# Performance work log

Measured on AMD Instinct MI355X. Metric: run time of the kernel, lower is better.

The kernel has to match this reference:

```python
import jax, jax.numpy as jnp
import numpy as np

B, S, D = 1, 4096, 1024
H = 16
HD = D // H  # 64


def setup_inputs() -> dict:
    key = jax.random.key(0)
    k1, k2, k3 = jax.random.split(key, 3)
    x = jax.random.normal(k1, (B, S, D), dtype=jnp.float32)
    W_qkv = jax.random.normal(k2, (D, 3 * D), dtype=jnp.float32) * (1.0 / np.sqrt(D))
    b_qkv = jnp.zeros((3 * D,), dtype=jnp.float32)
    W_out = jax.random.normal(k3, (D, D), dtype=jnp.float32) * (1.0 / np.sqrt(D))
    b_out = jnp.zeros((D,), dtype=jnp.float32)
    return {"x": x, "W_qkv": W_qkv, "b_qkv": b_qkv, "W_out": W_out, "b_out": b_out}


def reference(x, W_qkv, b_qkv, W_out, b_out):
    b, s, d = x.shape
    qkv = x @ W_qkv + b_qkv                      # [b, s, 3d]
    q, k, v = jnp.split(qkv, 3, axis=-1)
    q = q.reshape(b, s, H, HD)
    k = k.reshape(b, s, H, HD)
    v = v.reshape(b, s, H, HD)
    scale = 1.0 / np.sqrt(HD).astype(np.float32)
    scores = jnp.einsum("bqhd,bkhd->bhqk", q, k) * scale  # [b, h, s, s]
    causal = jnp.tril(jnp.ones((s, s), dtype=bool))
    scores = jnp.where(causal, scores, jnp.float32(-jnp.inf))
    attn = jax.nn.softmax(scores, axis=-1)
    out = jnp.einsum("bhqk,bkhd->bqhd", attn, v).reshape(b, s, d)
    return out @ W_out + b_out
```

## Files before the change

kernel.cpp:

```cpp
#include <hip/hip_runtime.h>
#include <cstdint>
#include <cstddef>


typedef __attribute__((ext_vector_type(4))) float f32x4;
typedef __attribute__((ext_vector_type(16))) float f32x16;
typedef __attribute__((ext_vector_type(8))) short s16x8;
typedef __attribute__((ext_vector_type(4))) unsigned u32x4;

#define SM_SCALE_LOG2 0.18033688011112042f

#if __has_builtin(__builtin_amdgcn_exp2f)
#define EXP2(x) __builtin_amdgcn_exp2f(x)
#else
#define EXP2(x) exp2f(x)
#endif

static __device__ __forceinline__ short f2bf(float f) {
  unsigned u = __builtin_bit_cast(unsigned, f);
  u = (u + 0x7fffu + ((u >> 16) & 1u)) >> 16;
  return (short)u;
}

static __device__ __forceinline__ unsigned cvtpk(float lo, float hi) {
  unsigned r;
  asm("v_cvt_pk_bf16_f32 %0, %1, %2" : "=v"(r) : "v"(lo), "v"(hi));
  return r;
}

static __device__ __forceinline__ void plswap(unsigned& a, unsigned& b) {
#if __has_builtin(__builtin_amdgcn_permlane32_swap)
  auto r = __builtin_amdgcn_permlane32_swap((int)a, (int)b, false, false);
  unsigned tmp[2];
  __builtin_memcpy(tmp, &r, 8);
  a = tmp[0];
  b = tmp[1];
#else
  const unsigned xa = (unsigned)__shfl_xor((int)a, 32);
  const unsigned xb = (unsigned)__shfl_xor((int)b, 32);
  const bool hiL = (threadIdx.x & 32) != 0;
  const unsigned na = hiL ? xb : a;
  const unsigned nb = hiL ? b : xa;
  a = na;
  b = nb;
#endif
}

static __device__ __forceinline__ void gload16(const void* g, void* l) {
  __builtin_amdgcn_global_load_lds((const __attribute__((address_space(1))) void*)g,
                                   (__attribute__((address_space(3))) void*)l, 16, 0, 0);
}

#define MFMA32(A, B, C) __builtin_amdgcn_mfma_f32_32x32x16_bf16(A, B, C, 0, 0, 0)

__global__ __launch_bounds__(256) void convx_k(const float* __restrict__ x,
                                               short* __restrict__ xb) {
  const size_t i = ((size_t)blockIdx.x * 256 + threadIdx.x) * 8;
  float4 a = *(const float4*)(x + i);
  float4 b = *(const float4*)(x + i + 4);
  u32x4 p;
  p[0] = cvtpk(a.x, a.y); p[1] = cvtpk(a.z, a.w);
  p[2] = cvtpk(b.x, b.y); p[3] = cvtpk(b.z, b.w);
  *(u32x4*)(xb + i) = p;
}

__global__ __launch_bounds__(256, 2) void convT_k(const float* __restrict__ W,
                                                  short* __restrict__ Wt, int K, int N) {
  __shared__ short T[64][72];
  const int t = threadIdx.x;
  const int n0 = blockIdx.x * 64, k0 = blockIdx.y * 64;
  const int kr = t >> 2, c0 = (t & 3) * 16;
  const float* src = W + (size_t)(k0 + kr) * N + n0 + c0;
  float4 v0 = *(const float4*)(src + 0);
  float4 v1 = *(const float4*)(src + 4);
  float4 v2 = *(const float4*)(src + 8);
  float4 v3 = *(const float4*)(src + 12);
  T[c0 + 0][kr] = f2bf(v0.x);  T[c0 + 1][kr] = f2bf(v0.y);
  T[c0 + 2][kr] = f2bf(v0.z);  T[c0 + 3][kr] = f2bf(v0.w);
  T[c0 + 4][kr] = f2bf(v1.x);  T[c0 + 5][kr] = f2bf(v1.y);
  T[c0 + 6][kr] = f2bf(v1.z);  T[c0 + 7][kr] = f2bf(v1.w);
  T[c0 + 8][kr] = f2bf(v2.x);  T[c0 + 9][kr] = f2bf(v2.y);
  T[c0 + 10][kr] = f2bf(v2.z); T[c0 + 11][kr] = f2bf(v2.w);
  T[c0 + 12][kr] = f2bf(v3.x); T[c0 + 13][kr] = f2bf(v3.y);
  T[c0 + 14][kr] = f2bf(v3.z); T[c0 + 15][kr] = f2bf(v3.w);
  __syncthreads();
  const int nr = t >> 2, kc = (t & 3) * 16;
  s16x8 a = *(const s16x8*)&T[nr][kc];
  s16x8 b = *(const s16x8*)&T[nr][kc + 8];
  short* dst = Wt + (size_t)(n0 + nr) * K + k0 + kc;
  *(s16x8*)dst = a;
  *(s16x8*)(dst + 8) = b;
}

template <int ABF, int SCAT>
__global__ __launch_bounds__(256, 2) void gemm_k(
    const void* __restrict__ Ap, const short* __restrict__ Bt,
    const float* __restrict__ bias,
    short* __restrict__ q_ws, short* __restrict__ k_ws, short* __restrict__ vt_ws,
    float* __restrict__ out, int N, int K) {
  constexpr int LDA = ABF ? 32 : 40;
  __shared__ short As[2][128 * LDA];
  __shared__ short Bs[2][128 * 32];

  const int t = threadIdx.x, l = t & 63, w = t >> 6;
  const int wm = (w >> 1) * 64, wn = (w & 1) * 64;
  const int m0 = blockIdx.x * 128, n0 = blockIdx.y * 128;
  const int lr = l & 15, lh = l >> 4;

  f32x4 acc[4][4];
#pragma unroll
  for (int i = 0; i < 4; i++)
#pragma unroll
    for (int j = 0; j < 4; j++) acc[i][j] = (f32x4){0.f, 0.f, 0.f, 0.f};

  const int arow = t >> 1, ac0 = (t & 1) * 16;
  const int grow = l >> 2, gc0 = (l & 3) * 8;

  auto stage = [&](int b, int kt) {
    {
      const int r0 = w * 32;
      const short* s0 = Bt + (size_t)(n0 + r0 + grow) * K + kt + gc0;
      gload16(s0, &Bs[b][r0 * 32]);
      gload16(s0 + (size_t)16 * K, &Bs[b][(r0 + 16) * 32]);
    }
    if constexpr (ABF) {
      const int r0 = w * 32;
      const short* s0 = (const short*)Ap + (size_t)(m0 + r0 + grow) * K + kt + gc0;
      gload16(s0, &As[b][r0 * 32]);
      gload16(s0 + (size_t)16 * K, &As[b][(r0 + 16) * 32]);
    } else {
      const float* ap = (const float*)Ap + (size_t)(m0 + arow) * K + kt + ac0;
      float4 v0 = *(const float4*)(ap + 0);
      float4 v1 = *(const float4*)(ap + 4);
      float4 v2 = *(const float4*)(ap + 8);
      float4 v3 = *(const float4*)(ap + 12);
      u32x4 p0, p1;
      p0[0] = cvtpk(v0.x, v0.y); p0[1] = cvtpk(v0.z, v0.w);
      p0[2] = cvtpk(v1.x, v1.y); p0[3] = cvtpk(v1.z, v1.w);
      p1[0] = cvtpk(v2.x, v2.y); p1[1] = cvtpk(v2.z, v2.w);
      p1[2] = cvtpk(v3.x, v3.y); p1[3] = cvtpk(v3.z, v3.w);
      *(u32x4*)&As[b][arow * LDA + ac0] = p0;
      *(u32x4*)&As[b][arow * LDA + ac0 + 8] = p1;
    }
  };

  const int nt = K >> 5;
  stage(0, 0);
  __syncthreads();
  int cur = 0;
  for (int tt = 0; tt < nt; tt++) {
    if (tt + 1 < nt) stage(cur ^ 1, (tt + 1) * 32);
    s16x8 af[4], bfv[4];
#pragma unroll
    for (int mi = 0; mi < 4; mi++)
      af[mi] = *(const s16x8*)&As[cur][(wm + mi * 16 + lr) * LDA + lh * 8];
#pragma unroll
    for (int ni = 0; ni < 4; ni++)
      bfv[ni] = *(const s16x8*)&Bs[cur][(wn + ni * 16 + lr) * 32 + lh * 8];
#pragma unroll
    for (int mi = 0; mi < 4; mi++)
#pragma unroll
      for (int ni = 0; ni < 4; ni++)
        acc[mi][ni] = __builtin_amdgcn_mfma_f32_16x16x32_bf16(af[mi], bfv[ni],
                                                              acc[mi][ni], 0, 0, 0);
    __syncthreads();
    cur ^= 1;
  }

#pragma unroll
  for (int mi = 0; mi < 4; mi++) {
#pragma unroll
    for (int ni = 0; ni < 4; ni++) {
      const int gn = n0 + wn + ni * 16 + lr;
      const float bb = bias[gn];
      if constexpr (SCAT) {
        const int sect = gn >> 10, dd = gn & 1023, hh = dd >> 6, hd = dd & 63;
#pragma unroll
        for (int j = 0; j < 4; j++) {
          const int gm = m0 + wm + mi * 16 + lh * 4 + j;
          const short bv = f2bf(acc[mi][ni][j] + bb);
          if (sect == 0)
            q_ws[((size_t)hh * 4096 + gm) * 64 + hd] = bv;
          else if (sect == 1)
            k_ws[((size_t)hh * 4096 + gm) * 64 + (hd ^ ((gm & 7) << 3))] = bv;
          else
            vt_ws[((size_t)hh * 64 + hd) * 4096 + (gm ^ ((hd & 7) << 3))] = bv;
        }
      } else {
#pragma unroll
        for (int j = 0; j < 4; j++) {
          const int gm = m0 + wm + mi * 16 + lh * 4 + j;
          out[(size_t)gm * N + gn] = acc[mi][ni][j] + bb;
        }
      }
    }
  }
}

__global__ __launch_bounds__(256, 3) void attn_k(
    const short* __restrict__ q_ws, const short* __restrict__ k_ws,
    const short* __restrict__ vt_ws, short* __restrict__ o_ws) {
  __shared__ short Ks[2][64 * 64];
  __shared__ short Vts[2][64 * 64];
  __shared__ float accO[64][64];
  __shared__ float mls[2][2][64];

  const int tid = threadIdx.x, l = tid & 63, w = tid >> 6;
  const int sid = w & 1, kh = w >> 1;
  const int ql = l & 31, hi = l >> 5;
  const int lin = blockIdx.x;
  const int logical = (lin & 7) * 64 + (lin >> 3);
  const int pair = logical & 31;
  const int h = logical >> 5;
  const int gl8 = l >> 3, gc8 = (l & 7) * 8;

  auto run = [&](int qb) {
    const int q0w = qb + 32 * sid;
    const int qg = q0w + ql;
    const int nt = (qb >> 6) + 1;

    s16x8 qf[4];
    {
      const short* qp = q_ws + ((size_t)h * 4096 + qg) * 64 + hi * 8;
      qf[0] = *(const s16x8*)qp;
      qf[1] = *(const s16x8*)(qp + 16);
      qf[2] = *(const s16x8*)(qp + 32);
      qf[3] = *(const s16x8*)(qp + 48);
    }

    f32x16 po0, po1;
#pragma unroll
    for (int r = 0; r < 16; r++) { po0[r] = 0.f; po1[r] = 0.f; }
    float m = -1e30f, ls = 0.f;

    auto stage = [&](int b, int tt) {
      const short* kb = k_ws + ((size_t)h * 4096 + (size_t)tt * 64 + w * 16 + gl8) * 64 + gc8;
      gload16(kb, &Ks[b][w * 16 * 64]);
      gload16(kb + (size_t)8 * 64, &Ks[b][(w * 16 + 8) * 64]);
      const short* vb = vt_ws + ((size_t)h * 64 + w * 16 + gl8) * 4096 + (size_t)tt * 64 + gc8;
      gload16(vb, &Vts[b][w * 16 * 64]);
      gload16(vb + (size_t)8 * 4096, &Vts[b][(w * 16 + 8) * 64]);
    };

    stage(0, 0);
    __syncthreads();
    int cur = 0;
    for (int tt = 0; tt < nt; tt++) {
      if (tt + 1 < nt) stage(cur ^ 1, tt + 1);
      const int kv0w = tt * 64 + kh * 32;
      if (kv0w <= q0w + 31) {
        const int row = kh * 32 + ql;
        f32x16 sa;
#pragma unroll
        for (int r = 0; r < 16; r++) sa[r] = 0.f;
#pragma unroll
        for (int ks2 = 0; ks2 < 4; ks2++) {
          s16x8 kf = *(const s16x8*)&Ks[cur][row * 64 + ((ks2 * 16 + hi * 8) ^ ((ql & 7) << 3))];
          sa = MFMA32(kf, qf[ks2], sa);
        }
        if (kv0w + 31 > q0w) {
#pragma unroll
          for (int r = 0; r < 16; r++) {
            const int kvl = (r & 3) + 8 * (r >> 2) + 4 * hi;
            if (kv0w + kvl > qg) sa[r] = -3e38f;
          }
        }
        const float x0 = fmaxf(fmaxf(sa[0], sa[1]), fmaxf(sa[2], sa[3]));
        const float x1 = fmaxf(fmaxf(sa[4], sa[5]), fmaxf(sa[6], sa[7]));
        const float x2 = fmaxf(fmaxf(sa[8], sa[9]), fmaxf(sa[10], sa[11]));
        const float x3 = fmaxf(fmaxf(sa[12], sa[13]), fmaxf(sa[14], sa[15]));
        float pm = fmaxf(fmaxf(x0, x1), fmaxf(x2, x3));
        pm = fmaxf(pm, __shfl_xor(pm, 32));
        pm *= SM_SCALE_LOG2;
        if (!__all(pm <= m + 8.0f)) {
          const float nm = fmaxf(m, pm);
          const float corr = EXP2(m - nm);
          m = nm;
          ls *= corr;
#pragma unroll
          for (int r = 0; r < 16; r++) {
            const int qr = (r & 3) + 8 * (r >> 2) + 4 * hi;
            const float cq = __shfl(corr, qr);
            po0[r] *= cq;
            po1[r] *= cq;
          }
        }
        float e[16];
#pragma unroll
        for (int r = 0; r < 16; r++) e[r] = EXP2(__builtin_fmaf(sa[r], SM_SCALE_LOG2, -m));
        float rs = ((e[0] + e[1]) + (e[2] + e[3])) + ((e[4] + e[5]) + (e[6] + e[7])) +
                   (((e[8] + e[9]) + (e[10] + e[11])) + ((e[12] + e[13]) + (e[14] + e[15])));
        rs += __shfl_xor(rs, 32);
        ls += rs;
        unsigned pk0 = cvtpk(e[0], e[1]), pk1 = cvtpk(e[2], e[3]);
        unsigned pk2 = cvtpk(e[4], e[5]), pk3 = cvtpk(e[6], e[7]);
        unsigned pk4 = cvtpk(e[8], e[9]), pk5 = cvtpk(e[10], e[11]);
        unsigned pk6 = cvtpk(e[12], e[13]), pk7 = cvtpk(e[14], e[15]);
        plswap(pk0, pk2);
        plswap(pk1, pk3);
        plswap(pk4, pk6);
        plswap(pk5, pk7);
        const u32x4 pw0 = {pk0, pk1, pk2, pk3};
        const u32x4 pw1 = {pk4, pk5, pk6, pk7};
        const s16x8 pa0 = __builtin_bit_cast(s16x8, pw0);
        const s16x8 pa1 = __builtin_bit_cast(s16x8, pw1);
        const int kidx0 = (kh * 32 + hi * 8) ^ ((ql & 7) << 3);
        const int kidx1 = (kh * 32 + 16 + hi * 8) ^ ((ql & 7) << 3);
        s16x8 vf00 = *(const s16x8*)&Vts[cur][ql * 64 + kidx0];
        s16x8 vf01 = *(const s16x8*)&Vts[cur][ql * 64 + kidx1];
        s16x8 vf10 = *(const s16x8*)&Vts[cur][(32 + ql) * 64 + kidx0];
        s16x8 vf11 = *(const s16x8*)&Vts[cur][(32 + ql) * 64 + kidx1];
        po0 = MFMA32(pa0, vf00, po0);
        po0 = MFMA32(pa1, vf01, po0);
        po1 = MFMA32(pa0, vf10, po1);
        po1 = MFMA32(pa1, vf11, po1);
      }
      __syncthreads();
      cur ^= 1;
    }

    const int qloc = sid * 32 + ql;
    if (hi == 0) {
      mls[kh][0][qloc] = m;
      mls[kh][1][qloc] = ls;
    }
    __syncthreads();
    float er[16];
#pragma unroll
    for (int r = 0; r < 16; r++) {
      const int qr = sid * 32 + (r & 3) + 8 * (r >> 2) + 4 * hi;
      const float mt = fmaxf(mls[0][0][qr], mls[1][0][qr]);
      er[r] = EXP2(mls[kh][0][qr] - mt);
    }
    if (kh == 0) {
#pragma unroll
      for (int r = 0; r < 16; r++) {
        const int qr = sid * 32 + (r & 3) + 8 * (r >> 2) + 4 * hi;
        accO[qr][ql] = po0[r] * er[r];
        accO[qr][32 + ql] = po1[r] * er[r];
      }
    }
    __syncthreads();
    if (kh == 1) {
#pragma unroll
      for (int r = 0; r < 16; r++) {
        const int qr = sid * 32 + (r & 3) + 8 * (r >> 2) + 4 * hi;
        accO[qr][ql] += po0[r] * er[r];
        accO[qr][32 + ql] += po1[r] * er[r];
      }
    }
    __syncthreads();
    {
      const int qo = tid >> 2, d0 = (tid & 3) * 16;
      const float m0v = mls[0][0][qo], m1v = mls[1][0][qo];
      const float mt = fmaxf(m0v, m1v);
      const float lst = mls[0][1][qo] * EXP2(m0v - mt) + mls[1][1][qo] * EXP2(m1v - mt);
      const float inv = 1.0f / lst;
      const f32x4 a0 = *(const f32x4*)&accO[qo][d0];
      const f32x4 a1 = *(const f32x4*)&accO[qo][d0 + 4];
      const f32x4 a2 = *(const f32x4*)&accO[qo][d0 + 8];
      const f32x4 a3 = *(const f32x4*)&accO[qo][d0 + 12];
      s16x8 ov0, ov1;
      ov0[0] = f2bf(a0[0] * inv); ov0[1] = f2bf(a0[1] * inv);
      ov0[2] = f2bf(a0[2] * inv); ov0[3] = f2bf(a0[3] * inv);
      ov0[4] = f2bf(a1[0] * inv); ov0[5] = f2bf(a1[1] * inv);
      ov0[6] = f2bf(a1[2] * inv); ov0[7] = f2bf(a1[3] * inv);
      ov1[0] = f2bf(a2[0] * inv); ov1[1] = f2bf(a2[1] * inv);
      ov1[2] = f2bf(a2[2] * inv); ov1[3] = f2bf(a2[3] * inv);
      ov1[4] = f2bf(a3[0] * inv); ov1[5] = f2bf(a3[1] * inv);
      ov1[6] = f2bf(a3[2] * inv); ov1[7] = f2bf(a3[3] * inv);
      short* op = o_ws + (size_t)(qb + qo) * 1024 + h * 64 + d0;
      *(s16x8*)op = ov0;
      *(s16x8*)(op + 8) = ov1;
    }
    __syncthreads();
  };

  run(pair * 64);
  run((63 - pair) * 64);
}

extern "C" void kernel_launch(void* const* d_in, const int* in_sizes, int n_in,
                              void* d_out, int out_size, void* d_ws, size_t ws_size,
                              hipStream_t stream) {
  const float* x     = (const float*)d_in[0];
  const float* W_qkv = (const float*)d_in[1];
  const float* b_qkv = (const float*)d_in[2];
  const float* W_out = (const float*)d_in[3];
  const float* b_out = (const float*)d_in[4];
  float* out = (float*)d_out;

  short* R0    = (short*)d_ws;
  short* q_ws  = R0 + (size_t)4 * 1024 * 1024;
  short* k_ws  = q_ws + (size_t)4 * 1024 * 1024;
  short* vt_ws = k_ws + (size_t)4 * 1024 * 1024;
  short* Wo_t  = vt_ws;
  short* xbf   = vt_ws + (size_t)4 * 1024 * 1024;

  const bool big_ws = ws_size >= (size_t)40 * 1024 * 1024;

  convT_k<<<dim3(48, 16), 256, 0, stream>>>(W_qkv, R0, 1024, 3072);
  if (big_ws) {
    convx_k<<<2048, 256, 0, stream>>>(x, xbf);
    gemm_k<1, 1><<<dim3(32, 24), 256, 0, stream>>>(xbf, R0, b_qkv, q_ws, k_ws,
                                                   vt_ws, nullptr, 3072, 1024);
  } else {
    gemm_k<0, 1><<<dim3(32, 24), 256, 0, stream>>>(x, R0, b_qkv, q_ws, k_ws,
                                                   vt_ws, nullptr, 3072, 1024);
  }
  attn_k<<<512, 256, 0, stream>>>(q_ws, k_ws, vt_ws, R0);
  convT_k<<<dim3(16, 16), 256, 0, stream>>>(W_out, Wo_t, 1024, 1024);
  gemm_k<1, 0><<<dim3(32, 8), 256, 0, stream>>>(R0, Wo_t, b_out, nullptr, nullptr,
                                                nullptr, out, 1024, 1024);
}
```

Before: 218.8 us.

## Split attention into one query block per workgroup, alias LDS, narrow output GEMM tile

```diff
diff --git a/kernel.cpp b/kernel.cpp
--- a/kernel.cpp
+++ b/kernel.cpp
@@ -92,55 +92,45 @@
   *(s16x8*)(dst + 8) = b;
 }
 
-template <int ABF, int SCAT>
+template <int SCAT, int NI>
 __global__ __launch_bounds__(256, 2) void gemm_k(
-    const void* __restrict__ Ap, const short* __restrict__ Bt,
+    const short* __restrict__ Ap, const short* __restrict__ Bt,
     const float* __restrict__ bias,
     short* __restrict__ q_ws, short* __restrict__ k_ws, short* __restrict__ vt_ws,
     float* __restrict__ out, int N, int K) {
-  constexpr int LDA = ABF ? 32 : 40;
-  __shared__ short As[2][128 * LDA];
-  __shared__ short Bs[2][128 * 32];
+  constexpr int BN = NI * 32;
+  __shared__ short As[2][128 * 32];
+  __shared__ short Bs[2][BN * 32];
 
   const int t = threadIdx.x, l = t & 63, w = t >> 6;
-  const int wm = (w >> 1) * 64, wn = (w & 1) * 64;
-  const int m0 = blockIdx.x * 128, n0 = blockIdx.y * 128;
+  const int wm = (w >> 1) * 64, wn = (w & 1) * (NI * 16);
+  const int m0 = blockIdx.x * 128, n0 = blockIdx.y * BN;
   const int lr = l & 15, lh = l >> 4;
 
-  f32x4 acc[4][4];
+  f32x4 acc[4][NI];
 #pragma unroll
   for (int i = 0; i < 4; i++)
 #pragma unroll
-    for (int j = 0; j < 4; j++) acc[i][j] = (f32x4){0.f, 0.f, 0.f, 0.f};
-
-  const int arow = t >> 1, ac0 = (t & 1) * 16;
+    for (int j = 0; j < NI; j++) acc[i][j] = (f32x4){0.f, 0.f, 0.f, 0.f};
+
   const int grow = l >> 2, gc0 = (l & 3) * 8;
 
   auto stage = [&](int b, int kt) {
-    {
+    if constexpr (NI == 4) {
       const int r0 = w * 32;
       const short* s0 = Bt + (size_t)(n0 + r0 + grow) * K + kt + gc0;
       gload16(s0, &Bs[b][r0 * 32]);
       gload16(s0 + (size_t)16 * K, &Bs[b][(r0 + 16) * 32]);
-    }
-    if constexpr (ABF) {
+    } else {
+      const int r0 = w * 16;
+      const short* s0 = Bt + (size_t)(n0 + r0 + grow) * K + kt + gc0;
+      gload16(s0, &Bs[b][r0 * 32]);
+    }
+    {
       const int r0 = w * 32;
-      const short* s0 = (const short*)Ap + (size_t)(m0 + r0 + grow) * K + kt + gc0;
+      const short* s0 = Ap + (size_t)(m0 + r0 + grow) * K + kt + gc0;
       gload16(s0, &As[b][r0 * 32]);
       gload16(s0 + (size_t)16 * K, &As[b][(r0 + 16) * 32]);
-    } else {
-      const float* ap = (const float*)Ap + (size_t)(m0 + arow) * K + kt + ac0;
-      float4 v0 = *(const float4*)(ap + 0);
-      float4 v1 = *(const float4*)(ap + 4);
-      float4 v2 = *(const float4*)(ap + 8);
-      float4 v3 = *(const float4*)(ap + 12);
-      u32x4 p0, p1;
-      p0[0] = cvtpk(v0.x, v0.y); p0[1] = cvtpk(v0.z, v0.w);
-      p0[2] = cvtpk(v1.x, v1.y); p0[3] = cvtpk(v1.z, v1.w);
-      p1[0] = cvtpk(v2.x, v2.y); p1[1] = cvtpk(v2.z, v2.w);
-      p1[2] = cvtpk(v3.x, v3.y); p1[3] = cvtpk(v3.z, v3.w);
-      *(u32x4*)&As[b][arow * LDA + ac0] = p0;
-      *(u32x4*)&As[b][arow * LDA + ac0 + 8] = p1;
     }
   };
 
@@ -150,17 +140,17 @@
   int cur = 0;
   for (int tt = 0; tt < nt; tt++) {
     if (tt + 1 < nt) stage(cur ^ 1, (tt + 1) * 32);
-    s16x8 af[4], bfv[4];
+    s16x8 af[4], bfv[NI];
 #pragma unroll
     for (int mi = 0; mi < 4; mi++)
-      af[mi] = *(const s16x8*)&As[cur][(wm + mi * 16 + lr) * LDA + lh * 8];
-#pragma unroll
-    for (int ni = 0; ni < 4; ni++)
+      af[mi] = *(const s16x8*)&As[cur][(wm + mi * 16 + lr) * 32 + lh * 8];
+#pragma unroll
+    for (int ni = 0; ni < NI; ni++)
       bfv[ni] = *(const s16x8*)&Bs[cur][(wn + ni * 16 + lr) * 32 + lh * 8];
 #pragma unroll
     for (int mi = 0; mi < 4; mi++)
 #pragma unroll
-      for (int ni = 0; ni < 4; ni++)
+      for (int ni = 0; ni < NI; ni++)
         acc[mi][ni] = __builtin_amdgcn_mfma_f32_16x16x32_bf16(af[mi], bfv[ni],
                                                               acc[mi][ni], 0, 0, 0);
     __syncthreads();
@@ -170,7 +160,7 @@
 #pragma unroll
   for (int mi = 0; mi < 4; mi++) {
 #pragma unroll
-    for (int ni = 0; ni < 4; ni++) {
+    for (int ni = 0; ni < NI; ni++) {
       const int gn = n0 + wn + ni * 16 + lr;
       const float bb = bias[gn];
       if constexpr (SCAT) {
@@ -197,187 +187,192 @@
   }
 }
 
-__global__ __launch_bounds__(256, 3) void attn_k(
+__global__ __launch_bounds__(256, 4) void attn_k(
     const short* __restrict__ q_ws, const short* __restrict__ k_ws,
     const short* __restrict__ vt_ws, short* __restrict__ o_ws) {
   __shared__ short Ks[2][64 * 64];
   __shared__ short Vts[2][64 * 64];
-  __shared__ float accO[64][64];
   __shared__ float mls[2][2][64];
+  float* accO = (float*)&Ks[0][0];
 
   const int tid = threadIdx.x, l = tid & 63, w = tid >> 6;
   const int sid = w & 1, kh = w >> 1;
   const int ql = l & 31, hi = l >> 5;
   const int lin = blockIdx.x;
-  const int logical = (lin & 7) * 64 + (lin >> 3);
-  const int pair = logical & 31;
-  const int h = logical >> 5;
+  const int j = lin & 15;
+  const int h = 2 * (j & 7) + (j >> 3);
+  const int i4 = lin >> 4;
+  int qbi;
+  switch (i4 >> 4) {
+    case 0: qbi = i4; break;
+    case 1: qbi = 79 - i4; break;
+    case 2: qbi = i4 - 16; break;
+    default: qbi = 95 - i4; break;
+  }
+  const int qb = qbi * 64;
+  const int q0w = qb + 32 * sid;
+  const int qg = q0w + ql;
+  const int nt = qbi + 1;
   const int gl8 = l >> 3, gc8 = (l & 7) * 8;
 
-  auto run = [&](int qb) {
-    const int q0w = qb + 32 * sid;
-    const int qg = q0w + ql;
-    const int nt = (qb >> 6) + 1;
-
-    s16x8 qf[4];
-    {
-      const short* qp = q_ws + ((size_t)h * 4096 + qg) * 64 + hi * 8;
-      qf[0] = *(const s16x8*)qp;
-      qf[1] = *(const s16x8*)(qp + 16);
-      qf[2] = *(const s16x8*)(qp + 32);
-      qf[3] = *(const s16x8*)(qp + 48);
-    }
-
-    f32x16 po0, po1;
-#pragma unroll
-    for (int r = 0; r < 16; r++) { po0[r] = 0.f; po1[r] = 0.f; }
-    float m = -1e30f, ls = 0.f;
-
-    auto stage = [&](int b, int tt) {
-      const short* kb = k_ws + ((size_t)h * 4096 + (size_t)tt * 64 + w * 16 + gl8) * 64 + gc8;
-      gload16(kb, &Ks[b][w * 16 * 64]);
-      gload16(kb + (size_t)8 * 64, &Ks[b][(w * 16 + 8) * 64]);
-      const short* vb = vt_ws + ((size_t)h * 64 + w * 16 + gl8) * 4096 + (size_t)tt * 64 + gc8;
-      gload16(vb, &Vts[b][w * 16 * 64]);
-      gload16(vb + (size_t)8 * 4096, &Vts[b][(w * 16 + 8) * 64]);
-    };
-
-    stage(0, 0);
+  s16x8 qf[4];
+  {
+    const short* qp = q_ws + ((size_t)h * 4096 + qg) * 64 + hi * 8;
+    qf[0] = *(const s16x8*)qp;
+    qf[1] = *(const s16x8*)(qp + 16);
+    qf[2] = *(const s16x8*)(qp + 32);
+    qf[3] = *(const s16x8*)(qp + 48);
+  }
+
+  f32x16 po0, po1;
+#pragma unroll
+  for (int r = 0; r < 16; r++) { po0[r] = 0.f; po1[r] = 0.f; }
+  float m = -1e30f, ls = 0.f;
+
+  auto stage = [&](int b, int tt) {
+    const short* kb = k_ws + ((size_t)h * 4096 + (size_t)tt * 64 + w * 16 + gl8) * 64 + gc8;
+    gload16(kb, &Ks[b][w * 16 * 64]);
+    gload16(kb + (size_t)8 * 64, &Ks[b][(w * 16 + 8) * 64]);
+    const short* vb = vt_ws + ((size_t)h * 64 + w * 16 + gl8) * 4096 + (size_t)tt * 64 + gc8;
+    gload16(vb, &Vts[b][w * 16 * 64]);
+    gload16(vb + (size_t)8 * 4096, &Vts[b][(w * 16 + 8) * 64]);
+  };
+
+  stage(0, 0);
+  __syncthreads();
+  int cur = 0;
+  for (int tt = 0; tt < nt; tt++) {
+    if (tt + 1 < nt) stage(cur ^ 1, tt + 1);
+    const int kv0w = tt * 64 + kh * 32;
+    if (kv0w <= q0w + 31) {
+      const int row = kh * 32 + ql;
+      f32x16 sa;
+#pragma unroll
+      for (int r = 0; r < 16; r++) sa[r] = 0.f;
+      __builtin_amdgcn_s_setprio(1);
+#pragma unroll
+      for (int ks2 = 0; ks2 < 4; ks2++) {
+        s16x8 kf = *(const s16x8*)&Ks[cur][row * 64 + ((ks2 * 16 + hi * 8) ^ ((ql & 7) << 3))];
+        sa = MFMA32(kf, qf[ks2], sa);
+      }
+      __builtin_amdgcn_s_setprio(0);
+      if (kv0w + 31 > q0w) {
+#pragma unroll
+        for (int r = 0; r < 16; r++) {
+          const int kvl = (r & 3) + 8 * (r >> 2) + 4 * hi;
+          if (kv0w + kvl > qg) sa[r] = -3e38f;
+        }
+      }
+      const float x0 = fmaxf(fmaxf(sa[0], sa[1]), fmaxf(sa[2], sa[3]));
+      const float x1 = fmaxf(fmaxf(sa[4], sa[5]), fmaxf(sa[6], sa[7]));
+      const float x2 = fmaxf(fmaxf(sa[8], sa[9]), fmaxf(sa[10], sa[11]));
+      const float x3 = fmaxf(fmaxf(sa[12], sa[13]), fmaxf(sa[14], sa[15]));
+      float pm = fmaxf(fmaxf(x0, x1), fmaxf(x2, x3));
+      pm = fmaxf(pm, __shfl_xor(pm, 32));
+      pm *= SM_SCALE_LOG2;
+      if (!__all(pm <= m + 8.0f)) {
+        const float nm = fmaxf(m, pm);
+        const float corr = EXP2(m - nm);
+        m = nm;
+        ls *= corr;
+#pragma unroll
+        for (int r = 0; r < 16; r++) {
+          const int qr = (r & 3) + 8 * (r >> 2) + 4 * hi;
+          const float cq = __shfl(corr, qr);
+          po0[r] *= cq;
+          po1[r] *= cq;
+        }
+      }
+      float e[16];
+#pragma unroll
+      for (int r = 0; r < 16; r++) e[r] = EXP2(__builtin_fmaf(sa[r], SM_SCALE_LOG2, -m));
+      float rs = ((e[0] + e[1]) + (e[2] + e[3])) + ((e[4] + e[5]) + (e[6] + e[7])) +
+                 (((e[8] + e[9]) + (e[10] + e[11])) + ((e[12] + e[13]) + (e[14] + e[15])));
+      rs += __shfl_xor(rs, 32);
+      ls += rs;
+      unsigned pk0 = cvtpk(e[0], e[1]), pk1 = cvtpk(e[2], e[3]);
+      unsigned pk2 = cvtpk(e[4], e[5]), pk3 = cvtpk(e[6], e[7]);
+      unsigned pk4 = cvtpk(e[8], e[9]), pk5 = cvtpk(e[10], e[11]);
+      unsigned pk6 = cvtpk(e[12], e[13]), pk7 = cvtpk(e[14], e[15]);
+      plswap(pk0, pk2);
+      plswap(pk1, pk3);
+      plswap(pk4, pk6);
+      plswap(pk5, pk7);
+      const u32x4 pw0 = {pk0, pk1, pk2, pk3};
+      const u32x4 pw1 = {pk4, pk5, pk6, pk7};
+      const s16x8 pa0 = __builtin_bit_cast(s16x8, pw0);
+      const s16x8 pa1 = __builtin_bit_cast(s16x8, pw1);
+      const int kidx0 = (kh * 32 + hi * 8) ^ ((ql & 7) << 3);
+      const int kidx1 = (kh * 32 + 16 + hi * 8) ^ ((ql & 7) << 3);
+      s16x8 vf00 = *(const s16x8*)&Vts[cur][ql * 64 + kidx0];
+      s16x8 vf01 = *(const s16x8*)&Vts[cur][ql * 64 + kidx1];
+      s16x8 vf10 = *(const s16x8*)&Vts[cur][(32 + ql) * 64 + kidx0];
+      s16x8 vf11 = *(const s16x8*)&Vts[cur][(32 + ql) * 64 + kidx1];
+      __builtin_amdgcn_s_setprio(1);
+      po0 = MFMA32(pa0, vf00, po0);
+      po0 = MFMA32(pa1, vf01, po0);
+      po1 = MFMA32(pa0, vf10, po1);
+      po1 = MFMA32(pa1, vf11, po1);
+      __builtin_amdgcn_s_setprio(0);
+    }
     __syncthreads();
-    int cur = 0;
-    for (int tt = 0; tt < nt; tt++) {
-      if (tt + 1 < nt) stage(cur ^ 1, tt + 1);
-      const int kv0w = tt * 64 + kh * 32;
-      if (kv0w <= q0w + 31) {
-        const int row = kh * 32 + ql;
-        f32x16 sa;
-#pragma unroll
-        for (int r = 0; r < 16; r++) sa[r] = 0.f;
-#pragma unroll
-        for (int ks2 = 0; ks2 < 4; ks2++) {
-          s16x8 kf = *(const s16x8*)&Ks[cur][row * 64 + ((ks2 * 16 + hi * 8) ^ ((ql & 7) << 3))];
-          sa = MFMA32(kf, qf[ks2], sa);
-        }
-        if (kv0w + 31 > q0w) {
-#pragma unroll
-          for (int r = 0; r < 16; r++) {
-            const int kvl = (r & 3) + 8 * (r >> 2) + 4 * hi;
-            if (kv0w + kvl > qg) sa[r] = -3e38f;
-          }
-        }
-        const float x0 = fmaxf(fmaxf(sa[0], sa[1]), fmaxf(sa[2], sa[3]));
-        const float x1 = fmaxf(fmaxf(sa[4], sa[5]), fmaxf(sa[6], sa[7]));
-        const float x2 = fmaxf(fmaxf(sa[8], sa[9]), fmaxf(sa[10], sa[11]));
-        const float x3 = fmaxf(fmaxf(sa[12], sa[13]), fmaxf(sa[14], sa[15]));
-        float pm = fmaxf(fmaxf(x0, x1), fmaxf(x2, x3));
-        pm = fmaxf(pm, __shfl_xor(pm, 32));
-        pm *= SM_SCALE_LOG2;
-        if (!__all(pm <= m + 8.0f)) {
-          const float nm = fmaxf(m, pm);
-          const float corr = EXP2(m - nm);
-          m = nm;
-          ls *= corr;
-#pragma unroll
-          for (int r = 0; r < 16; r++) {
-            const int qr = (r & 3) + 8 * (r >> 2) + 4 * hi;
-            const float cq = __shfl(corr, qr);
-            po0[r] *= cq;
-            po1[r] *= cq;
-          }
-        }
-        float e[16];
-#pragma unroll
-        for (int r = 0; r < 16; r++) e[r] = EXP2(__builtin_fmaf(sa[r], SM_SCALE_LOG2, -m));
-        float rs = ((e[0] + e[1]) + (e[2] + e[3])) + ((e[4] + e[5]) + (e[6] + e[7])) +
-                   (((e[8] + e[9]) + (e[10] + e[11])) + ((e[12] + e[13]) + (e[14] + e[15])));
-        rs += __shfl_xor(rs, 32);
-        ls += rs;
-        unsigned pk0 = cvtpk(e[0], e[1]), pk1 = cvtpk(e[2], e[3]);
-        unsigned pk2 = cvtpk(e[4], e[5]), pk3 = cvtpk(e[6], e[7]);
-        unsigned pk4 = cvtpk(e[8], e[9]), pk5 = cvtpk(e[10], e[11]);
-        unsigned pk6 = cvtpk(e[12], e[13]), pk7 = cvtpk(e[14], e[15]);
-        plswap(pk0, pk2);
-        plswap(pk1, pk3);
-        plswap(pk4, pk6);
-        plswap(pk5, pk7);
-        const u32x4 pw0 = {pk0, pk1, pk2, pk3};
-        const u32x4 pw1 = {pk4, pk5, pk6, pk7};
-        const s16x8 pa0 = __builtin_bit_cast(s16x8, pw0);
-        const s16x8 pa1 = __builtin_bit_cast(s16x8, pw1);
-        const int kidx0 = (kh * 32 + hi * 8) ^ ((ql & 7) << 3);
-        const int kidx1 = (kh * 32 + 16 + hi * 8) ^ ((ql & 7) << 3);
-        s16x8 vf00 = *(const s16x8*)&Vts[cur][ql * 64 + kidx0];
-        s16x8 vf01 = *(const s16x8*)&Vts[cur][ql * 64 + kidx1];
-        s16x8 vf10 = *(const s16x8*)&Vts[cur][(32 + ql) * 64 + kidx0];
-        s16x8 vf11 = *(const s16x8*)&Vts[cur][(32 + ql) * 64 + kidx1];
-        po0 = MFMA32(pa0, vf00, po0);
-        po0 = MFMA32(pa1, vf01, po0);
-        po1 = MFMA32(pa0, vf10, po1);
-        po1 = MFMA32(pa1, vf11, po1);
-      }
-      __syncthreads();
-      cur ^= 1;
-    }
-
-    const int qloc = sid * 32 + ql;
-    if (hi == 0) {
-      mls[kh][0][qloc] = m;
-      mls[kh][1][qloc] = ls;
-    }
-    __syncthreads();
-    float er[16];
+    cur ^= 1;
+  }
+
+  const int qloc = sid * 32 + ql;
+  if (hi == 0) {
+    mls[kh][0][qloc] = m;
+    mls[kh][1][qloc] = ls;
+  }
+  __syncthreads();
+  float er[16];
+#pragma unroll
+  for (int r = 0; r < 16; r++) {
+    const int qr = sid * 32 + (r & 3) + 8 * (r >> 2) + 4 * hi;
+    const float mt = fmaxf(mls[0][0][qr], mls[1][0][qr]);
+    er[r] = EXP2(mls[kh][0][qr] - mt);
+  }
+  if (kh == 0) {
 #pragma unroll
     for (int r = 0; r < 16; r++) {
       const int qr = sid * 32 + (r & 3) + 8 * (r >> 2) + 4 * hi;
-      const float mt = fmaxf(mls[0][0][qr], mls[1][0][qr]);
-      er[r] = EXP2(mls[kh][0][qr] - mt);
-    }
-    if (kh == 0) {
-#pragma unroll
-      for (int r = 0; r < 16; r++) {
-        const int qr = sid * 32 + (r & 3) + 8 * (r >> 2) + 4 * hi;
-        accO[qr][ql] = po0[r] * er[r];
-        accO[qr][32 + ql] = po1[r] * er[r];
-      }
-    }
-    __syncthreads();
-    if (kh == 1) {
-#pragma unroll
-      for (int r = 0; r < 16; r++) {
-        const int qr = sid * 32 + (r & 3) + 8 * (r >> 2) + 4 * hi;
-        accO[qr][ql] += po0[r] * er[r];
-        accO[qr][32 + ql] += po1[r] * er[r];
-      }
-    }
-    __syncthreads();
-    {
-      const int qo = tid >> 2, d0 = (tid & 3) * 16;
-      const float m0v = mls[0][0][qo], m1v = mls[1][0][qo];
-      const float mt = fmaxf(m0v, m1v);
-      const float lst = mls[0][1][qo] * EXP2(m0v - mt) + mls[1][1][qo] * EXP2(m1v - mt);
-      const float inv = 1.0f / lst;
-      const f32x4 a0 = *(const f32x4*)&accO[qo][d0];
-      const f32x4 a1 = *(const f32x4*)&accO[qo][d0 + 4];
-      const f32x4 a2 = *(const f32x4*)&accO[qo][d0 + 8];
-      const f32x4 a3 = *(const f32x4*)&accO[qo][d0 + 12];
-      s16x8 ov0, ov1;
-      ov0[0] = f2bf(a0[0] * inv); ov0[1] = f2bf(a0[1] * inv);
-      ov0[2] = f2bf(a0[2] * inv); ov0[3] = f2bf(a0[3] * inv);
-      ov0[4] = f2bf(a1[0] * inv); ov0[5] = f2bf(a1[1] * inv);
-      ov0[6] = f2bf(a1[2] * inv); ov0[7] = f2bf(a1[3] * inv);
-      ov1[0] = f2bf(a2[0] * inv); ov1[1] = f2bf(a2[1] * inv);
-      ov1[2] = f2bf(a2[2] * inv); ov1[3] = f2bf(a2[3] * inv);
-      ov1[4] = f2bf(a3[0] * inv); ov1[5] = f2bf(a3[1] * inv);
-      ov1[6] = f2bf(a3[2] * inv); ov1[7] = f2bf(a3[3] * inv);
-      short* op = o_ws + (size_t)(qb + qo) * 1024 + h * 64 + d0;
-      *(s16x8*)op = ov0;
-      *(s16x8*)(op + 8) = ov1;
-    }
-    __syncthreads();
-  };
-
-  run(pair * 64);
-  run((63 - pair) * 64);
+      accO[qr * 64 + ql] = po0[r] * er[r];
+      accO[qr * 64 + 32 + ql] = po1[r] * er[r];
+    }
+  }
+  __syncthreads();
+  if (kh == 1) {
+#pragma unroll
+    for (int r = 0; r < 16; r++) {
+      const int qr = sid * 32 + (r & 3) + 8 * (r >> 2) + 4 * hi;
+      accO[qr * 64 + ql] += po0[r] * er[r];
+      accO[qr * 64 + 32 + ql] += po1[r] * er[r];
+    }
+  }
+  __syncthreads();
+  {
+    const int qo = tid >> 2, d0 = (tid & 3) * 16;
+    const float m0v = mls[0][0][qo], m1v = mls[1][0][qo];
+    const float mt = fmaxf(m0v, m1v);
+    const float lst = mls[0][1][qo] * EXP2(m0v - mt) + mls[1][1][qo] * EXP2(m1v - mt);
+    const float inv = 1.0f / lst;
+    const f32x4 a0 = *(const f32x4*)&accO[qo * 64 + d0];
+    const f32x4 a1 = *(const f32x4*)&accO[qo * 64 + d0 + 4];
+    const f32x4 a2 = *(const f32x4*)&accO[qo * 64 + d0 + 8];
+    const f32x4 a3 = *(const f32x4*)&accO[qo * 64 + d0 + 12];
+    s16x8 ov0, ov1;
+    ov0[0] = f2bf(a0[0] * inv); ov0[1] = f2bf(a0[1] * inv);
+    ov0[2] = f2bf(a0[2] * inv); ov0[3] = f2bf(a0[3] * inv);
+    ov0[4] = f2bf(a1[0] * inv); ov0[5] = f2bf(a1[1] * inv);
+    ov0[6] = f2bf(a1[2] * inv); ov0[7] = f2bf(a1[3] * inv);
+    ov1[0] = f2bf(a2[0] * inv); ov1[1] = f2bf(a2[1] * inv);
+    ov1[2] = f2bf(a2[2] * inv); ov1[3] = f2bf(a2[3] * inv);
+    ov1[4] = f2bf(a3[0] * inv); ov1[5] = f2bf(a3[1] * inv);
+    ov1[6] = f2bf(a3[2] * inv); ov1[7] = f2bf(a3[3] * inv);
+    short* op = o_ws + (size_t)(qb + qo) * 1024 + h * 64 + d0;
+    *(s16x8*)op = ov0;
+    *(s16x8*)(op + 8) = ov1;
+  }
 }
 
 extern "C" void kernel_launch(void* const* d_in, const int* in_sizes, int n_in,
@@ -395,21 +390,14 @@
   short* k_ws  = q_ws + (size_t)4 * 1024 * 1024;
   short* vt_ws = k_ws + (size_t)4 * 1024 * 1024;
   short* Wo_t  = vt_ws;
-  short* xbf   = vt_ws + (size_t)4 * 1024 * 1024;
-
-  const bool big_ws = ws_size >= (size_t)40 * 1024 * 1024;
-
+  short* xbf   = (short*)d_out;
+
+  convx_k<<<2048, 256, 0, stream>>>(x, xbf);
   convT_k<<<dim3(48, 16), 256, 0, stream>>>(W_qkv, R0, 1024, 3072);
-  if (big_ws) {
-    convx_k<<<2048, 256, 0, stream>>>(x, xbf);
-    gemm_k<1, 1><<<dim3(32, 24), 256, 0, stream>>>(xbf, R0, b_qkv, q_ws, k_ws,
-                                                   vt_ws, nullptr, 3072, 1024);
-  } else {
-    gemm_k<0, 1><<<dim3(32, 24), 256, 0, stream>>>(x, R0, b_qkv, q_ws, k_ws,
-                                                   vt_ws, nullptr, 3072, 1024);
-  }
-  attn_k<<<512, 256, 0, stream>>>(q_ws, k_ws, vt_ws, R0);
+  gemm_k<1, 4><<<dim3(32, 24), 256, 0, stream>>>(xbf, R0, b_qkv, q_ws, k_ws,
+                                                 vt_ws, nullptr, 3072, 1024);
+  attn_k<<<1024, 256, 0, stream>>>(q_ws, k_ws, vt_ws, R0);
   convT_k<<<dim3(16, 16), 256, 0, stream>>>(W_out, Wo_t, 1024, 1024);
-  gemm_k<1, 0><<<dim3(32, 8), 256, 0, stream>>>(R0, Wo_t, b_out, nullptr, nullptr,
-                                                nullptr, out, 1024, 1024);
-}
+  gemm_k<0, 2><<<dim3(32, 16), 256, 0, stream>>>(R0, Wo_t, b_out, nullptr,
+                                                 nullptr, nullptr, out, 1024, 1024);
+}
```

Measured after the change: 212.3 us. 1.03x faster.
